# Optimization experiments

Hardware: AMD Instinct MI355X
Metric: run time of the kernel (lower is better)

## Reference

```python
import jax, jax.numpy as jnp
import numpy as np

# irreps_in = irreps_out = 64x0e + 32x1o
MUL0, MUL1 = 64, 32          # multiplicities of 0e scalars and 1o vectors
DIM_IN = MUL0 + MUL1 * 3     # 160
N_NODES = 50000
IU0, IV0 = np.triu_indices(MUL0, k=1)   # 2016 scalar u<v pairs
IU1, IV1 = np.triu_indices(MUL1, k=1)   # 496 vector u<v pairs
# e3nn path normalization (component / element):
#   i_out=0 (0e): num_elements sum = 2016 + 64 + 496 + 32 = 2608, dim(0e)=1
#   i_out=1 (1o): num_elements = 32*64 = 2048, dim(1o)=3
C0 = float(np.sqrt(1.0 / 2608.0))
C1 = float(np.sqrt(3.0 / 2048.0))
INV_SQRT3 = float(1.0 / np.sqrt(3.0))   # w3j(1,0,1) and w3j(1,1,0) CG factor


def setup_inputs() -> dict:
    key = jax.random.key(0)
    ks = jax.random.split(key, 7)
    node_feats = jax.random.normal(ks[0], (N_NODES, DIM_IN), jnp.float32)
    node_messages = jax.random.normal(ks[1], (N_NODES, DIM_IN), jnp.float32)
    W1 = jax.random.normal(ks[2], (len(IU0), MUL0), jnp.float32)  # (0e,0e)->0e u<vw
    W2 = jax.random.normal(ks[3], (MUL0, MUL0), jnp.float32)      # (0e,0e)->0e uuw
    W3 = jax.random.normal(ks[4], (MUL1, MUL0, MUL1), jnp.float32)  # (1o,0e)->1o uvw
    W4 = jax.random.normal(ks[5], (len(IU1), MUL0), jnp.float32)  # (1o,1o)->0e u<vw
    W5 = jax.random.normal(ks[6], (MUL1, MUL0), jnp.float32)      # (1o,1o)->0e uuw
    return {"node_feats": node_feats, "node_messages": node_messages,
            "W1": W1, "W2": W2, "W3": W3, "W4": W4, "W5": W5}


def _tensor_square(x, W1, W2, W3, W4, W5):
    x0 = x[:, :MUL0]                        # [N, 64] scalars (0e)
    x1 = x[:, MUL0:].reshape(-1, MUL1, 3)   # [N, 32, 3] vectors (1o)
    # (0e x 0e) -> 0e
    pair0 = x0[:, IU0] * x0[:, IV0]         # [N, 2016]
    sq0 = x0 * x0                           # [N, 64]
    # (1o x 1o) -> 0e via dot products (w3j(1,1,0) = delta/sqrt3)
    d = jnp.einsum('nui,nvi->nuv', x1, x1)  # [N, 32, 32]
    pair1 = d[:, IU1, IV1] * INV_SQRT3      # [N, 496]
    diag1 = jnp.einsum('nui,nui->nu', x1, x1) * INV_SQRT3  # [N, 32]
    out0 = C0 * (pair0 @ W1 + sq0 @ W2 + pair1 @ W4 + diag1 @ W5)  # [N, 64]
    # (1o x 0e) -> 1o fully connected uvw (w3j(1,0,1) = eye/sqrt3)
    out1 = (C1 * INV_SQRT3) * jnp.einsum('nui,nv,uvw->nwi', x1, x0, W3)  # [N,32,3]
    return jnp.concatenate([out0, out1.reshape(-1, MUL1 * 3)], axis=1)


def reference(node_feats, node_messages, W1, W2, W3, W4, W5):
    x = node_feats + node_messages
    return _tensor_square(x, W1, W2, W3, W4, W5)
```

## Files before the change

kernel.cpp:

```cpp
#include <hip/hip_runtime.h>
#include <math.h>

typedef unsigned short u16;
typedef unsigned int u32;

#define N_NODES 50000
#define NB      64

#define BG_OFF  0
#define BT_OFF  262144
#define BH_OFF  327680

#define ASTR   72
#define AHSTR  40
#define XTSTR  68

typedef __attribute__((ext_vector_type(8))) short short8;
typedef __attribute__((ext_vector_type(4))) float f32x4;
union U4S8 { uint4 u; short8 s; };

__device__ __forceinline__ u16 f2bf(float f) {
    u32 u = __float_as_uint(f);
    return (u16)((u + 0x7fffu + ((u >> 16) & 1u)) >> 16);
}
__device__ __forceinline__ f32x4 bf4(uint2 q) {
    f32x4 r;
    r[0] = __uint_as_float(q.x << 16);
    r[1] = __uint_as_float(q.x & 0xffff0000u);
    r[2] = __uint_as_float(q.y << 16);
    r[3] = __uint_as_float(q.y & 0xffff0000u);
    return r;
}

__device__ __forceinline__ int gslot(int u, int v, int w) {
    int j = u * 64 + w;
    return (j >> 4) * 1024 + (v >> 5) * 512 + (((v >> 3) & 3) * 16 + (j & 15)) * 8 + (v & 7);
}
__device__ __forceinline__ int tslot(int u, int v, int w) {
    int j = u * 32 + w;
    return (j >> 4) * 1024 + (v >> 5) * 512 + (((v >> 3) & 3) * 16 + (j & 15)) * 8 + (v & 7);
}
__device__ __forceinline__ int hslot(int u, int v, int w) {
    int j = u * 64 + w;
    return (j >> 4) * 512 + (((v >> 3) & 3) * 16 + (j & 15)) * 8 + (v & 7);
}

#define PA (2016 * 64)
#define PB (64 * 64)
#define PC (2048 * 32)
#define PD (496 * 64)
#define PE (32 * 64)
#define PTOT (PA + PB + PC + PD + PE)

__global__ __launch_bounds__(256)
void pack_kernel(const float* __restrict__ W1, const float* __restrict__ W2,
                 const float* __restrict__ W3, const float* __restrict__ W4,
                 const float* __restrict__ W5, u16* __restrict__ ws) {
    const float INV_SQRT3 = 0.57735026918962576f;
    int T = blockIdx.x * 256 + threadIdx.x;
    if (T < PA) {
        int p = T >> 6, w = T & 63;
        u16 bv = f2bf(0.5f * W1[T]);
        int a = (int)((127.0f - sqrtf(16129.0f - 8.0f * (float)p)) * 0.5f);
        a = max(0, min(a, 62));
        while (a > 0 && p < a * (127 - a) / 2) --a;
        while (p >= (a + 1) * (126 - a) / 2) ++a;
        int b = a + 1 + (p - a * (127 - a) / 2);
        ws[BG_OFF + gslot(b, a, w)] = bv;
        ws[BG_OFF + gslot(a, b, w)] = bv;
    } else if (T < PA + PB) {
        int t = T - PA;
        int v = t >> 6, w = t & 63;
        ws[BG_OFF + gslot(v, v, w)] = f2bf(W2[t]);
    } else if (T < PA + PB + PC) {
        int t = T - PA - PB;
        int k = t >> 5, w = t & 31;
        int u = k >> 6, v = k & 63;
        ws[BT_OFF + tslot(u, v, w)] = f2bf(W3[t]);
    } else if (T < PA + PB + PC + PD) {
        int t = T - PA - PB - PC;
        int p = t >> 6, w = t & 63;
        u16 bv = f2bf(0.5f * INV_SQRT3 * W4[t]);
        int a = (int)((63.0f - sqrtf(3969.0f - 8.0f * (float)p)) * 0.5f);
        a = max(0, min(a, 30));
        while (a > 0 && p < a * (63 - a) / 2) --a;
        while (p >= (a + 1) * (62 - a) / 2) ++a;
        int b = a + 1 + (p - a * (63 - a) / 2);
        ws[BH_OFF + hslot(b, a, w)] = bv;
        ws[BH_OFF + hslot(a, b, w)] = bv;
    } else if (T < PTOT) {
        int t = T - PA - PB - PC - PD;
        int v = t >> 6, w = t & 63;
        ws[BH_OFF + hslot(v, v, w)] = f2bf(INV_SQRT3 * W5[t]);
    }
}

__global__ __launch_bounds__(256, 3)
void node_block_kernel(const float* __restrict__ feats, const float* __restrict__ msgs,
                       const u16* __restrict__ ws, float* __restrict__ out) {
    __shared__ u16 A_S[64 * ASTR];
    __shared__ u16 A_H[192 * AHSTR];
    __shared__ u16 x0T[64 * XTSTR];
    __shared__ u16 x1T[96 * XTSTR];

    const int tid = threadIdx.x;
    const int node0 = blockIdx.x * NB;

    for (int k = 0; k < 5; ++k) {
        int chunk = tid + k * 256;
        int idx = chunk * 8;
        int n = (u32)idx / 160u;
        int d = idx - n * 160;
        int g = node0 * 160 + idx;
        float v[8];
        if (g + 8 <= N_NODES * 160) {
            float4 fa0 = *(const float4*)(feats + g);
            float4 fa1 = *(const float4*)(feats + g + 4);
            float4 fb0 = *(const float4*)(msgs + g);
            float4 fb1 = *(const float4*)(msgs + g + 4);
            v[0]=fa0.x+fb0.x; v[1]=fa0.y+fb0.y; v[2]=fa0.z+fb0.z; v[3]=fa0.w+fb0.w;
            v[4]=fa1.x+fb1.x; v[5]=fa1.y+fb1.y; v[6]=fa1.z+fb1.z; v[7]=fa1.w+fb1.w;
        } else {
            #pragma unroll
            for (int j = 0; j < 8; ++j) v[j] = 0.f;
        }
        u16 bv[8];
        #pragma unroll
        for (int j = 0; j < 8; ++j) bv[j] = f2bf(v[j]);
        if (d < 64) {
            uint4 pk;
            pk.x = ((u32)bv[1] << 16) | bv[0];
            pk.y = ((u32)bv[3] << 16) | bv[2];
            pk.z = ((u32)bv[5] << 16) | bv[4];
            pk.w = ((u32)bv[7] << 16) | bv[6];
            *(uint4*)&A_S[n * ASTR + d] = pk;
            #pragma unroll
            for (int j = 0; j < 8; ++j) x0T[(d + j) * XTSTR + n] = bv[j];
        } else {
            #pragma unroll
            for (int j = 0; j < 8; ++j) {
                int dd = d + j - 64;
                int u = (u32)dd / 3u, i = dd - u * 3;
                A_H[(i * 64 + n) * AHSTR + u] = bv[j];
                x1T[(u * 3 + i) * XTSTR + n] = bv[j];
            }
        }
    }
    __syncthreads();

    const int wave = tid >> 6, lane = tid & 63, quad = lane >> 4, l15 = lane & 15;
    const int wq = wave;
    const f32x4 z4 = {0.f, 0.f, 0.f, 0.f};

    f32x4 o0[4];
    #pragma unroll
    for (int mt = 0; mt < 4; ++mt) o0[mt] = z4;

    {
        short8 aS[4][2];
        #pragma unroll
        for (int mt = 0; mt < 4; ++mt)
            #pragma unroll
            for (int ks = 0; ks < 2; ++ks) {
                U4S8 t; t.u = *(const uint4*)&A_S[(mt * 16 + l15) * ASTR + ks * 32 + quad * 8];
                aS[mt][ks] = t.s;
            }
        const u16* bp = ws + BG_OFF + (u32)wq * 1024 + lane * 8;
        U4S8 b0[2], b1[2];
        b0[0].u = *(const uint4*)(bp);
        b1[0].u = *(const uint4*)(bp + 512);
        b0[1].u = *(const uint4*)(bp + 4096);
        b1[1].u = *(const uint4*)(bp + 4096 + 512);
        #pragma unroll 2
        for (int u = 0; u < 64; ++u) {
            const int c = u & 1;
            short8 B0 = b0[c].s, B1 = b1[c].s;
            if (u < 62) {
                b0[c].u = *(const uint4*)(bp + (u + 2) * 4096);
                b1[c].u = *(const uint4*)(bp + (u + 2) * 4096 + 512);
            }
            f32x4 acc[4];
            #pragma unroll
            for (int mt = 0; mt < 4; ++mt) acc[mt] = z4;
            #pragma unroll
            for (int mt = 0; mt < 4; ++mt)
                acc[mt] = __builtin_amdgcn_mfma_f32_16x16x32_bf16(aS[mt][0], B0, acc[mt], 0, 0, 0);
            #pragma unroll
            for (int mt = 0; mt < 4; ++mt)
                acc[mt] = __builtin_amdgcn_mfma_f32_16x16x32_bf16(aS[mt][1], B1, acc[mt], 0, 0, 0);
            #pragma unroll
            for (int mt = 0; mt < 4; ++mt) {
                f32x4 xq = bf4(*(const uint2*)&x0T[u * XTSTR + mt * 16 + quad * 4]);
                o0[mt] += xq * acc[mt];
            }
        }
    }

    #pragma unroll 1
    for (int i = 0; i < 3; ++i) {
        short8 aH[4];
        #pragma unroll
        for (int m = 0; m < 4; ++m) {
            U4S8 t; t.u = *(const uint4*)&A_H[((i * 4 + m) * 16 + l15) * AHSTR + quad * 8];
            aH[m] = t.s;
        }
        const u16* bp = ws + BH_OFF + (u32)wq * 512 + lane * 8;
        U4S8 bc, bn;
        bc.u = *(const uint4*)(bp);
        #pragma unroll 1
        for (int u = 0; u < 32; ++u) {
            if (u < 31) bn.u = *(const uint4*)(bp + 2048); else bn = bc;
            bp += 2048;
            f32x4 acc[4];
            #pragma unroll
            for (int m = 0; m < 4; ++m) acc[m] = z4;
            #pragma unroll
            for (int m = 0; m < 4; ++m)
                acc[m] = __builtin_amdgcn_mfma_f32_16x16x32_bf16(aH[m], bc.s, acc[m], 0, 0, 0);
            #pragma unroll
            for (int m = 0; m < 4; ++m) {
                f32x4 xq = bf4(*(const uint2*)&x1T[(u * 3 + i) * XTSTR + m * 16 + quad * 4]);
                o0[m] += xq * acc[m];
            }
            bc = bn;
        }
    }

    {
        const float C0v = 0.019581512f;
        #pragma unroll
        for (int mt = 0; mt < 4; ++mt)
            #pragma unroll
            for (int rr = 0; rr < 4; ++rr) {
                int node = node0 + mt * 16 + quad * 4 + rr;
                if (node < N_NODES)
                    out[node * 160 + wq * 16 + l15] = C0v * o0[mt][rr];
            }
    }

    {
        const int mh = wave >> 1, wh = wave & 1;
        short8 aT[2][2];
        #pragma unroll
        for (int m = 0; m < 2; ++m)
            #pragma unroll
            for (int ks = 0; ks < 2; ++ks) {
                U4S8 t; t.u = *(const uint4*)&A_S[((mh * 2 + m) * 16 + l15) * ASTR + ks * 32 + quad * 8];
                aT[m][ks] = t.s;
            }
        f32x4 o1[3][2];
        #pragma unroll
        for (int i = 0; i < 3; ++i)
            #pragma unroll
            for (int m = 0; m < 2; ++m) o1[i][m] = z4;

        const u16* bp = ws + BT_OFF + (u32)wh * 1024 + lane * 8;
        U4S8 b0[2], b1[2];
        b0[0].u = *(const uint4*)(bp);
        b1[0].u = *(const uint4*)(bp + 512);
        b0[1].u = *(const uint4*)(bp + 2048);
        b1[1].u = *(const uint4*)(bp + 2048 + 512);
        #pragma unroll 2
        for (int u = 0; u < 32; ++u) {
            const int c = u & 1;
            short8 B0 = b0[c].s, B1 = b1[c].s;
            if (u < 30) {
                b0[c].u = *(const uint4*)(bp + (u + 2) * 2048);
                b1[c].u = *(const uint4*)(bp + (u + 2) * 2048 + 512);
            }
            f32x4 acc[2];
            #pragma unroll
            for (int m = 0; m < 2; ++m) acc[m] = z4;
            #pragma unroll
            for (int m = 0; m < 2; ++m)
                acc[m] = __builtin_amdgcn_mfma_f32_16x16x32_bf16(aT[m][0], B0, acc[m], 0, 0, 0);
            #pragma unroll
            for (int m = 0; m < 2; ++m)
                acc[m] = __builtin_amdgcn_mfma_f32_16x16x32_bf16(aT[m][1], B1, acc[m], 0, 0, 0);
            #pragma unroll
            for (int i = 0; i < 3; ++i)
                #pragma unroll
                for (int m = 0; m < 2; ++m) {
                    f32x4 xq = bf4(*(const uint2*)&x1T[(u * 3 + i) * XTSTR + (mh * 2 + m) * 16 + quad * 4]);
                    o1[i][m] += xq * acc[m];
                }
        }
        const float S1 = 0.022097087f;
        #pragma unroll
        for (int i = 0; i < 3; ++i)
            #pragma unroll
            for (int m = 0; m < 2; ++m)
                #pragma unroll
                for (int rr = 0; rr < 4; ++rr) {
                    int node = node0 + (mh * 2 + m) * 16 + quad * 4 + rr;
                    if (node < N_NODES)
                        out[node * 160 + 64 + (wh * 16 + l15) * 3 + i] = S1 * o1[i][m][rr];
                }
    }
}

extern "C" void kernel_launch(void* const* d_in, const int* in_sizes, int n_in,
                              void* d_out, int out_size, void* d_ws, size_t ws_size,
                              hipStream_t stream) {
    const float* feats = (const float*)d_in[0];
    const float* msgs  = (const float*)d_in[1];
    const float* W1    = (const float*)d_in[2];
    const float* W2    = (const float*)d_in[3];
    const float* W3    = (const float*)d_in[4];
    const float* W4    = (const float*)d_in[5];
    const float* W5    = (const float*)d_in[6];
    float* out = (float*)d_out;
    u16* ws = (u16*)d_ws;

    hipLaunchKernelGGL(pack_kernel, dim3((PTOT + 255) / 256), dim3(256), 0, stream,
                       W1, W2, W3, W4, W5, ws);
    hipLaunchKernelGGL(node_block_kernel, dim3((N_NODES + NB - 1) / NB), dim3(256), 0, stream,
                       feats, msgs, ws, out);
}
```

Baseline: 204.3 us.

## Gather-pack weights per output slot, stagger weight traversal per block, merge i-loop

The weight pack kernel now writes each 8-element bf16 slot once with a vectorized store, gathering from W1..W5 by index instead of scattering with triangular-index inversion. The launch shrinks to 192 blocks. In the node kernel, each block starts its sweep over the weight tiles at a different phase (blockIdx*5), so concurrent blocks read different parts of the weight buffer and fewer of them hit the same L2 and memory channels at once. The vector-vector (A_H) path drops its outer i-loop: all 12 A fragments stay in registers and each B load is reused for three MFMA groups, with double buffering. This cuts B reloads but raises register pressure under the 3-blocks-per-CU launch bound.

```diff
diff --git a/kernel.cpp b/kernel.cpp
--- a/kernel.cpp
+++ b/kernel.cpp
@@ -1,5 +1,4 @@
 #include <hip/hip_runtime.h>
-#include <math.h>
 
 typedef unsigned short u16;
 typedef unsigned int u32;
@@ -32,67 +31,63 @@
     return r;
 }
 
-__device__ __forceinline__ int gslot(int u, int v, int w) {
-    int j = u * 64 + w;
-    return (j >> 4) * 1024 + (v >> 5) * 512 + (((v >> 3) & 3) * 16 + (j & 15)) * 8 + (v & 7);
-}
-__device__ __forceinline__ int tslot(int u, int v, int w) {
-    int j = u * 32 + w;
-    return (j >> 4) * 1024 + (v >> 5) * 512 + (((v >> 3) & 3) * 16 + (j & 15)) * 8 + (v & 7);
-}
-__device__ __forceinline__ int hslot(int u, int v, int w) {
-    int j = u * 64 + w;
-    return (j >> 4) * 512 + (((v >> 3) & 3) * 16 + (j & 15)) * 8 + (v & 7);
-}
-
-#define PA (2016 * 64)
-#define PB (64 * 64)
-#define PC (2048 * 32)
-#define PD (496 * 64)
-#define PE (32 * 64)
-#define PTOT (PA + PB + PC + PD + PE)
-
 __global__ __launch_bounds__(256)
 void pack_kernel(const float* __restrict__ W1, const float* __restrict__ W2,
                  const float* __restrict__ W3, const float* __restrict__ W4,
                  const float* __restrict__ W5, u16* __restrict__ ws) {
     const float INV_SQRT3 = 0.57735026918962576f;
     int T = blockIdx.x * 256 + threadIdx.x;
-    if (T < PA) {
-        int p = T >> 6, w = T & 63;
-        u16 bv = f2bf(0.5f * W1[T]);
-        int a = (int)((127.0f - sqrtf(16129.0f - 8.0f * (float)p)) * 0.5f);
-        a = max(0, min(a, 62));
-        while (a > 0 && p < a * (127 - a) / 2) --a;
-        while (p >= (a + 1) * (126 - a) / 2) ++a;
-        int b = a + 1 + (p - a * (127 - a) / 2);
-        ws[BG_OFF + gslot(b, a, w)] = bv;
-        ws[BG_OFF + gslot(a, b, w)] = bv;
-    } else if (T < PA + PB) {
-        int t = T - PA;
-        int v = t >> 6, w = t & 63;
-        ws[BG_OFF + gslot(v, v, w)] = f2bf(W2[t]);
-    } else if (T < PA + PB + PC) {
-        int t = T - PA - PB;
-        int k = t >> 5, w = t & 31;
-        int u = k >> 6, v = k & 63;
-        ws[BT_OFF + tslot(u, v, w)] = f2bf(W3[t]);
-    } else if (T < PA + PB + PC + PD) {
-        int t = T - PA - PB - PC;
-        int p = t >> 6, w = t & 63;
-        u16 bv = f2bf(0.5f * INV_SQRT3 * W4[t]);
-        int a = (int)((63.0f - sqrtf(3969.0f - 8.0f * (float)p)) * 0.5f);
-        a = max(0, min(a, 30));
-        while (a > 0 && p < a * (63 - a) / 2) --a;
-        while (p >= (a + 1) * (62 - a) / 2) ++a;
-        int b = a + 1 + (p - a * (63 - a) / 2);
-        ws[BH_OFF + hslot(b, a, w)] = bv;
-        ws[BH_OFF + hslot(a, b, w)] = bv;
-    } else if (T < PTOT) {
-        int t = T - PA - PB - PC - PD;
-        int v = t >> 6, w = t & 63;
-        ws[BH_OFF + hslot(v, v, w)] = f2bf(INV_SQRT3 * W5[t]);
-    }
+    int slot0 = T * 8;
+    float vals[8];
+    if (slot0 < BT_OFF) {
+        int ntile = slot0 >> 10, rem = slot0 & 1023;
+        int ks = rem >> 9, q = (rem & 511) >> 3;
+        int vbase = ks * 32 + (q >> 4) * 8;
+        int j = ntile * 16 + (q & 15);
+        int u = j >> 6, w = j & 63;
+        #pragma unroll
+        for (int jj = 0; jj < 8; ++jj) {
+            int v = vbase + jj;
+            if (v == u) vals[jj] = W2[u * 64 + w];
+            else {
+                int a = min(u, v), b = max(u, v);
+                int p = a * (127 - a) / 2 + (b - a - 1);
+                vals[jj] = 0.5f * W1[p * 64 + w];
+            }
+        }
+    } else if (slot0 < BH_OFF) {
+        int s = slot0 - BT_OFF;
+        int ntile = s >> 10, rem = s & 1023;
+        int ks = rem >> 9, q = (rem & 511) >> 3;
+        int vbase = ks * 32 + (q >> 4) * 8;
+        int j = ntile * 16 + (q & 15);
+        int u = j >> 5, w = j & 31;
+        #pragma unroll
+        for (int jj = 0; jj < 8; ++jj)
+            vals[jj] = W3[(u * 64 + (vbase + jj)) * 32 + w];
+    } else {
+        int s = slot0 - BH_OFF;
+        int ntile = s >> 9, q = (s & 511) >> 3;
+        int vbase = (q >> 4) * 8;
+        int j = ntile * 16 + (q & 15);
+        int u = j >> 6, w = j & 63;
+        #pragma unroll
+        for (int jj = 0; jj < 8; ++jj) {
+            int v = vbase + jj;
+            if (v == u) vals[jj] = W5[u * 64 + w] * INV_SQRT3;
+            else {
+                int a = min(u, v), b = max(u, v);
+                int p = a * (63 - a) / 2 + (b - a - 1);
+                vals[jj] = (0.5f * INV_SQRT3) * W4[p * 64 + w];
+            }
+        }
+    }
+    uint4 o;
+    o.x = ((u32)f2bf(vals[1]) << 16) | f2bf(vals[0]);
+    o.y = ((u32)f2bf(vals[3]) << 16) | f2bf(vals[2]);
+    o.z = ((u32)f2bf(vals[5]) << 16) | f2bf(vals[4]);
+    o.w = ((u32)f2bf(vals[7]) << 16) | f2bf(vals[6]);
+    *(uint4*)(ws + slot0) = o;
 }
 
 __global__ __launch_bounds__(256, 3)
@@ -151,6 +146,8 @@
     const int wave = tid >> 6, lane = tid & 63, quad = lane >> 4, l15 = lane & 15;
     const int wq = wave;
     const f32x4 z4 = {0.f, 0.f, 0.f, 0.f};
+    const int ph64 = (blockIdx.x * 5) & 63;
+    const int ph32 = (blockIdx.x * 5) & 31;
 
     f32x4 o0[4];
     #pragma unroll
@@ -167,17 +164,22 @@
             }
         const u16* bp = ws + BG_OFF + (u32)wq * 1024 + lane * 8;
         U4S8 b0[2], b1[2];
-        b0[0].u = *(const uint4*)(bp);
-        b1[0].u = *(const uint4*)(bp + 512);
-        b0[1].u = *(const uint4*)(bp + 4096);
-        b1[1].u = *(const uint4*)(bp + 4096 + 512);
+        b0[0].u = *(const uint4*)(bp + ph64 * 4096);
+        b1[0].u = *(const uint4*)(bp + ph64 * 4096 + 512);
+        {
+            int p1 = ((ph64 + 1) & 63) * 4096;
+            b0[1].u = *(const uint4*)(bp + p1);
+            b1[1].u = *(const uint4*)(bp + p1 + 512);
+        }
         #pragma unroll 2
-        for (int u = 0; u < 64; ++u) {
-            const int c = u & 1;
+        for (int t = 0; t < 64; ++t) {
+            const int c = t & 1;
+            const int u = (ph64 + t) & 63;
             short8 B0 = b0[c].s, B1 = b1[c].s;
-            if (u < 62) {
-                b0[c].u = *(const uint4*)(bp + (u + 2) * 4096);
-                b1[c].u = *(const uint4*)(bp + (u + 2) * 4096 + 512);
+            if (t < 62) {
+                int pp = ((ph64 + t + 2) & 63) * 4096;
+                b0[c].u = *(const uint4*)(bp + pp);
+                b1[c].u = *(const uint4*)(bp + pp + 512);
             }
             f32x4 acc[4];
             #pragma unroll
@@ -196,33 +198,37 @@
         }
     }
 
-    #pragma unroll 1
-    for (int i = 0; i < 3; ++i) {
-        short8 aH[4];
-        #pragma unroll
-        for (int m = 0; m < 4; ++m) {
-            U4S8 t; t.u = *(const uint4*)&A_H[((i * 4 + m) * 16 + l15) * AHSTR + quad * 8];
+    {
+        short8 aH[12];
+        #pragma unroll
+        for (int m = 0; m < 12; ++m) {
+            U4S8 t; t.u = *(const uint4*)&A_H[(m * 16 + l15) * AHSTR + quad * 8];
             aH[m] = t.s;
         }
         const u16* bp = ws + BH_OFF + (u32)wq * 512 + lane * 8;
-        U4S8 bc, bn;
-        bc.u = *(const uint4*)(bp);
-        #pragma unroll 1
-        for (int u = 0; u < 32; ++u) {
-            if (u < 31) bn.u = *(const uint4*)(bp + 2048); else bn = bc;
-            bp += 2048;
-            f32x4 acc[4];
-            #pragma unroll
-            for (int m = 0; m < 4; ++m) acc[m] = z4;
-            #pragma unroll
-            for (int m = 0; m < 4; ++m)
-                acc[m] = __builtin_amdgcn_mfma_f32_16x16x32_bf16(aH[m], bc.s, acc[m], 0, 0, 0);
-            #pragma unroll
-            for (int m = 0; m < 4; ++m) {
-                f32x4 xq = bf4(*(const uint2*)&x1T[(u * 3 + i) * XTSTR + m * 16 + quad * 4]);
-                o0[m] += xq * acc[m];
-            }
-            bc = bn;
+        U4S8 bb[2];
+        bb[0].u = *(const uint4*)(bp + ph32 * 2048);
+        bb[1].u = *(const uint4*)(bp + ((ph32 + 1) & 31) * 2048);
+        #pragma unroll 2
+        for (int t = 0; t < 32; ++t) {
+            const int c = t & 1;
+            const int u = (ph32 + t) & 31;
+            short8 B = bb[c].s;
+            if (t < 30) bb[c].u = *(const uint4*)(bp + ((ph32 + t + 2) & 31) * 2048);
+            #pragma unroll
+            for (int i = 0; i < 3; ++i) {
+                f32x4 acc[4];
+                #pragma unroll
+                for (int m = 0; m < 4; ++m) acc[m] = z4;
+                #pragma unroll
+                for (int m = 0; m < 4; ++m)
+                    acc[m] = __builtin_amdgcn_mfma_f32_16x16x32_bf16(aH[i * 4 + m], B, acc[m], 0, 0, 0);
+                #pragma unroll
+                for (int m = 0; m < 4; ++m) {
+                    f32x4 xq = bf4(*(const uint2*)&x1T[(u * 3 + i) * XTSTR + m * 16 + quad * 4]);
+                    o0[m] += xq * acc[m];
+                }
+            }
         }
     }
 
@@ -256,17 +262,22 @@
 
         const u16* bp = ws + BT_OFF + (u32)wh * 1024 + lane * 8;
         U4S8 b0[2], b1[2];
-        b0[0].u = *(const uint4*)(bp);
-        b1[0].u = *(const uint4*)(bp + 512);
-        b0[1].u = *(const uint4*)(bp + 2048);
-        b1[1].u = *(const uint4*)(bp + 2048 + 512);
+        b0[0].u = *(const uint4*)(bp + ph32 * 2048);
+        b1[0].u = *(const uint4*)(bp + ph32 * 2048 + 512);
+        {
+            int p1 = ((ph32 + 1) & 31) * 2048;
+            b0[1].u = *(const uint4*)(bp + p1);
+            b1[1].u = *(const uint4*)(bp + p1 + 512);
+        }
         #pragma unroll 2
-        for (int u = 0; u < 32; ++u) {
-            const int c = u & 1;
+        for (int t = 0; t < 32; ++t) {
+            const int c = t & 1;
+            const int u = (ph32 + t) & 31;
             short8 B0 = b0[c].s, B1 = b1[c].s;
-            if (u < 30) {
-                b0[c].u = *(const uint4*)(bp + (u + 2) * 2048);
-                b1[c].u = *(const uint4*)(bp + (u + 2) * 2048 + 512);
+            if (t < 30) {
+                int pp = ((ph32 + t + 2) & 31) * 2048;
+                b0[c].u = *(const uint4*)(bp + pp);
+                b1[c].u = *(const uint4*)(bp + pp + 512);
             }
             f32x4 acc[2];
             #pragma unroll
@@ -312,7 +323,7 @@
     float* out = (float*)d_out;
     u16* ws = (u16*)d_ws;
 
-    hipLaunchKernelGGL(pack_kernel, dim3((PTOT + 255) / 256), dim3(256), 0, stream,
+    hipLaunchKernelGGL(pack_kernel, dim3(192), dim3(256), 0, stream,
                        W1, W2, W3, W4, W5, ws);
     hipLaunchKernelGGL(node_block_kernel, dim3((N_NODES + NB - 1) / NB), dim3(256), 0, stream,
                        feats, msgs, ws, out);
```

Measured after the change: 197.8 us. 1.03x faster.
